# Optimization experiments

Measured on AMD Instinct MI355X. Metric: run time of the kernel, lower is better.

The kernel has to match this reference:

```python
import jax, jax.numpy as jnp
import numpy as np

N = 768
INPUT_DIM = 128
HIDDEN = 256
HEADS = 8
HEAD_DIM = HIDDEN // HEADS  # 32
SCALE = float(np.sqrt(HEAD_DIM))


def _linear_params(key, fan_in, fan_out):
    kw, kb = jax.random.split(key)
    lim = 1.0 / np.sqrt(fan_in)
    W = jax.random.uniform(kw, (fan_in, fan_out), jnp.float32, -lim, lim)
    b = jax.random.uniform(kb, (fan_out,), jnp.float32, -lim, lim)
    return W, b


def setup_inputs() -> dict:
    key = jax.random.key(0)
    ks = jax.random.split(key, 9)
    x = jax.random.normal(ks[0], (N, INPUT_DIM), jnp.float32)
    pos = jax.random.normal(ks[1], (N, 3), jnp.float32)
    Wq, bq = _linear_params(ks[2], INPUT_DIM, HIDDEN)
    Wk, bk = _linear_params(ks[3], INPUT_DIM, HIDDEN)
    Wv, bv = _linear_params(ks[4], INPUT_DIM, HIDDEN)
    Wo, bo = _linear_params(ks[5], HIDDEN, HIDDEN)
    W1, b1 = _linear_params(ks[6], 3, HIDDEN)
    W2, b2 = _linear_params(ks[7], HIDDEN, HIDDEN)
    W3, b3 = _linear_params(ks[8], HIDDEN, HEAD_DIM)
    return dict(x=x, pos=pos, Wq=Wq, bq=bq, Wk=Wk, bk=bk, Wv=Wv, bv=bv,
                Wo=Wo, bo=bo, W1=W1, b1=b1, W2=W2, b2=b2, W3=W3, b3=b3)


def reference(x, pos, Wq, bq, Wk, bk, Wv, bv, Wo, bo, W1, b1, W2, b2, W3, b3):
    n = x.shape[0]
    Q = (x @ Wq + bq).reshape(n, HEADS, HEAD_DIM)
    K = (x @ Wk + bk).reshape(n, HEADS, HEAD_DIM)
    V = (x @ Wv + bv).reshape(n, HEADS, HEAD_DIM)

    # rel_pos[i, j] = pos[j] - pos[i], shape (N, N, 3)
    rel = pos[None, :, :] - pos[:, None, :]
    h = jax.nn.relu(rel @ W1 + b1)          # (N, N, HIDDEN)
    h = jax.nn.relu(h @ W2 + b2)            # (N, N, HIDDEN)
    enc = h @ W3 + b3                        # (N, N, HEAD_DIM)

    scores = jnp.einsum('ihd,jhd->hij', Q, K) / SCALE
    scores = scores + jnp.einsum('ihd,ijd->hij', Q, enc) / SCALE
    attn = jax.nn.softmax(scores, axis=-1)   # (H, N, N); dropout is identity at eval
    out = jnp.einsum('hij,jhd->ihd', attn, V).reshape(n, HIDDEN)
    return out @ Wo + bo
```

## Files before the change

### kernel.cpp

```cpp
#include <hip/hip_runtime.h>
#include <hip/hip_bf16.h>

#define N 768
#define IN_DIM 128
#define HID 256
#define HD 32
#define TJ 64
#define NT (N / TJ)
#define NTH (NT / 2)
#define SCALE_INV 0.17677669529663687f

typedef short s16x8 __attribute__((ext_vector_type(8)));
typedef float f32x4 __attribute__((ext_vector_type(4)));

__device__ __forceinline__ float bf2f(unsigned short s) {
    return __uint_as_float(((unsigned)s) << 16);
}
__device__ __forceinline__ unsigned short bf_bits(float f) {
    __hip_bfloat16 h = __float2bfloat16(f);
    union { __hip_bfloat16 h; unsigned short u; } c; c.h = h; return c.u;
}
__device__ __forceinline__ unsigned cvt2(float a, float b) {
    __hip_bfloat162 h2 = __float22bfloat162_rn(make_float2(a, b));
    union { __hip_bfloat162 h; unsigned u; } c; c.h = h2; return c.u;
}

#define BAR_LDS() do { asm volatile("s_waitcnt lgkmcnt(0)" ::: "memory"); \
                       __builtin_amdgcn_s_barrier(); } while (0)

__global__ __launch_bounds__(256) void prep_kernel(
    const float* __restrict__ x, const float* __restrict__ pos,
    const float* __restrict__ Wq, const float* __restrict__ bq,
    const float* __restrict__ Wk, const float* __restrict__ bk,
    const float* __restrict__ Wv, const float* __restrict__ bv,
    const float* __restrict__ W1, const float* __restrict__ W2,
    const float* __restrict__ W3, const float* __restrict__ Wo,
    float* __restrict__ Q, float* __restrict__ Kt,
    unsigned short* __restrict__ Vt, float* __restrict__ A,
    unsigned short* __restrict__ w2f, float* __restrict__ WoT,
    unsigned short* __restrict__ w3qg)
{
    const int bx = blockIdx.x, t = threadIdx.x;
    __shared__ float xs[IN_DIM];
    __shared__ float ps[3];
    __shared__ float qrow[HID];

    if (bx >= N) {
        const int p = (bx - N) * 256 + t;
        const int e = p & 7, l = (p >> 3) & 63, nt = (p >> 9) & 15, s = p >> 13;
        const int krow = 32 * s + 8 * (l >> 4) + e;
        const int ncol = 16 * nt + (l & 15);
        w2f[p] = bf_bits(W2[krow * HID + ncol]);
        WoT[p] = Wo[(p & 255) * HID + (p >> 8)];
        return;
    }

    const int i = bx;
    if (t < IN_DIM) xs[t] = x[i * IN_DIM + t];
    if (t < 3) ps[t] = pos[i * 3 + t];
    __syncthreads();
    float q = bq[t], k = bk[t], v = bv[t];
#pragma unroll 8
    for (int kk = 0; kk < IN_DIM; ++kk) {
        const float xv = xs[kk];
        q += xv * Wq[kk * HID + t];
        k += xv * Wk[kk * HID + t];
        v += xv * Wv[kk * HID + t];
    }
    const float a = ps[0] * W1[t] + ps[1] * W1[HID + t] + ps[2] * W1[2 * HID + t];
    Q[i * HID + t] = q;
    Kt[(size_t)t * N + i] = k;
    Vt[(size_t)t * N + i] = bf_bits(v);
    A[i * HID + t] = a;
    qrow[t] = q;
    __syncthreads();

    const int l = t & 63, sp = t >> 6, lg = l >> 4, hh = l & 15;
#pragma unroll
    for (int ss = 0; ss < 2; ++ss) {
        const int s = 2 * sp + ss;
        s16x8 frag = {0, 0, 0, 0, 0, 0, 0, 0};
        if (hh < 8) {
#pragma unroll
            for (int e = 0; e < 8; ++e) {
                const int kk = 32 * s + 8 * lg + e;
                const float* w3p = W3 + kk * HD;
                float acc = 0.f;
#pragma unroll
                for (int d0 = 0; d0 < 32; d0 += 4) {
                    const float4 wv = *(const float4*)(w3p + d0);
                    acc += wv.x * qrow[hh * HD + d0] + wv.y * qrow[hh * HD + d0 + 1]
                         + wv.z * qrow[hh * HD + d0 + 2] + wv.w * qrow[hh * HD + d0 + 3];
                }
                frag[e] = (short)bf_bits(acc);
            }
        }
        *(s16x8*)(w3qg + (size_t)i * 4096 + (size_t)(s * 64 + l) * 8) = frag;
    }
}

__global__ __launch_bounds__(256) void s1_kernel(
    const float* __restrict__ Q, const float* __restrict__ Kt,
    float* __restrict__ S1)
{
    const int t = threadIdx.x;
    const int i0 = (blockIdx.x / 12) * 32;
    const int j0 = (blockIdx.x % 12) * 64;
    __shared__ float qTs[256 * 36];

    {
        const int iq = t & 31;
        const int dbase = (t >> 5) * 32;
        const int xk = t >> 5;
        const int colsw = (((iq >> 2) ^ xk) << 2) + (iq & 3);
        const float* qp = Q + (size_t)(i0 + iq) * HID + dbase;
#pragma unroll
        for (int cc = 0; cc < 8; ++cc) {
            const float4 qv = *(const float4*)(qp + 4 * cc);
            qTs[(dbase + 4 * cc + 0) * 36 + colsw] = qv.x;
            qTs[(dbase + 4 * cc + 1) * 36 + colsw] = qv.y;
            qTs[(dbase + 4 * cc + 2) * 36 + colsw] = qv.z;
            qTs[(dbase + 4 * cc + 3) * 36 + colsw] = qv.w;
        }
    }
    __syncthreads();

    const int h = t >> 5, jj = t & 31;
    const int j1 = j0 + jj, j2 = j0 + jj + 32;
    f32x4 acc0[8] = {}, acc1[8] = {};
    const float* kp = Kt + (size_t)(32 * h) * N + j1;
#pragma unroll 4
    for (int d = 0; d < 32; ++d) {
        const float k0 = kp[(size_t)d * N];
        const float k1 = kp[(size_t)d * N + 32];
        const float* qrow = &qTs[(32 * h + d) * 36];
#pragma unroll
        for (int ic = 0; ic < 8; ++ic) {
            const f32x4 qv = *(const f32x4*)&qrow[(ic ^ h) << 2];
            acc0[ic] += qv * k0;
            acc1[ic] += qv * k1;
        }
    }
    float* op = S1 + (size_t)h * (N * N) + (size_t)i0 * N;
#pragma unroll
    for (int ic = 0; ic < 8; ++ic)
#pragma unroll
        for (int u = 0; u < 4; ++u) {
            op[(size_t)(4 * ic + u) * N + j1] = acc0[ic][u];
            op[(size_t)(4 * ic + u) * N + j2] = acc1[ic][u];
        }
}

__global__ __launch_bounds__(256, 2) void fused_main_kernel(
    const float* __restrict__ Ag, const float* __restrict__ S1,
    const unsigned short* __restrict__ Vt,
    const unsigned short* __restrict__ w2fg, const unsigned short* __restrict__ w3qg,
    const float* __restrict__ b1, const float* __restrict__ b2,
    float* __restrict__ pv0g, float* __restrict__ pv1g,
    float* __restrict__ psump, float* __restrict__ mp)
{
    const int bid = blockIdx.x;
    const int i = bid >> 1, jhalf = bid & 1;
    const int t = threadIdx.x;
    const int w = t >> 6, l = t & 63;
    const int lg = l >> 4, l15 = l & 15;

    __shared__ __align__(16) short h1f[4 * 8 * 64 * 8];
    __shared__ __align__(16) short h2s[64 * 264];
    __shared__ __align__(16) short w3qf[8 * 64 * 8];
    __shared__ __align__(16) float slds[8 * 68];
    __shared__ __align__(16) float plds[8 * 68];
    __shared__ float basek[HID];
    __shared__ float hm[8], hpsum[8], hresc[8];

    basek[t] = b1[t] - Ag[(size_t)i * HID + t];
    {
        const int c0 = t, c1 = t + 256;
        *(s16x8*)&w3qf[c0 * 8] = *(const s16x8*)(w3qg + (size_t)i * 4096 + (size_t)c0 * 8);
        *(s16x8*)&w3qf[c1 * 8] = *(const s16x8*)(w3qg + (size_t)i * 4096 + (size_t)c1 * 8);
    }
    if (t < 8) { hm[t] = -3.0e38f; hpsum[t] = 0.f; }
    float bias[4];
#pragma unroll
    for (int n = 0; n < 4; ++n) bias[n] = b2[64 * w + 16 * n + l15];

    float pv = 0.f;
    const int hsel = w + ((l >> 5) << 2);
    const int hid2 = hsel * 32 + (l & 31);
    const unsigned short* vrow = Vt + (size_t)hid2 * N;
    BAR_LDS();

#pragma unroll 1
    for (int tt = 0; tt < NTH; ++tt) {
        const int j0 = (jhalf * NTH + tt) * TJ;

        const int jj = 16 * w + l15;
        const float* ap = Ag + (size_t)(j0 + jj) * HID + 8 * lg;
#pragma unroll
        for (int s = 0; s < 8; ++s) {
            const float4 a0 = *(const float4*)(ap + 32 * s);
            const float4 a1 = *(const float4*)(ap + 32 * s + 4);
            const float4 c0 = *(const float4*)&basek[32 * s + 8 * lg];
            const float4 c4 = *(const float4*)&basek[32 * s + 8 * lg + 4];
            uint4 hv;
            hv.x = cvt2(fmaxf(a0.x + c0.x, 0.f), fmaxf(a0.y + c0.y, 0.f));
            hv.y = cvt2(fmaxf(a0.z + c0.z, 0.f), fmaxf(a0.w + c0.w, 0.f));
            hv.z = cvt2(fmaxf(a1.x + c4.x, 0.f), fmaxf(a1.y + c4.y, 0.f));
            hv.w = cvt2(fmaxf(a1.z + c4.z, 0.f), fmaxf(a1.w + c4.w, 0.f));
            *(uint4*)&h1f[((w * 8 + s) * 64 + l) * 8] = hv;
        }
        float4 s1v = make_float4(0.f, 0.f, 0.f, 0.f);
        if (l15 < 8)
            s1v = *(const float4*)(S1 + (size_t)l15 * (N * N) + (size_t)i * N
                                   + j0 + 16 * w + 4 * lg);
        s16x8 bfr[32];
#pragma unroll
        for (int s = 0; s < 8; ++s)
#pragma unroll
            for (int n = 0; n < 4; ++n)
                bfr[s * 4 + n] = *(const s16x8*)(w2fg +
                    (size_t)(((s * 16 + 4 * w + n) * 64 + l)) * 8);
        BAR_LDS();

#pragma unroll
        for (int mt = 0; mt < 4; ++mt) {
            s16x8 a[8];
#pragma unroll
            for (int s = 0; s < 8; ++s)
                a[s] = *(const s16x8*)&h1f[((mt * 8 + s) * 64 + l) * 8];
#pragma unroll
            for (int n = 0; n < 4; ++n) {
                f32x4 acc = {bias[n], bias[n], bias[n], bias[n]};
#pragma unroll
                for (int s = 0; s < 8; ++s)
                    acc = __builtin_amdgcn_mfma_f32_16x16x32_bf16(a[s], bfr[s * 4 + n], acc, 0, 0, 0);
                const int col = 64 * w + 16 * n + l15;
                const int jrow = 16 * mt + 4 * lg;
#pragma unroll
                for (int r = 0; r < 4; ++r)
                    h2s[(jrow + r) * 264 + col] = (short)bf_bits(fmaxf(acc[r], 0.f));
            }
        }
        BAR_LDS();

        f32x4 acc2 = {};
#pragma unroll
        for (int s = 0; s < 8; ++s) {
            const s16x8 a2 = *(const s16x8*)&h2s[(16 * w + l15) * 264 + 32 * s + 8 * lg];
            const s16x8 wq = *(const s16x8*)&w3qf[(s * 64 + l) * 8];
            acc2 = __builtin_amdgcn_mfma_f32_16x16x32_bf16(a2, wq, acc2, 0, 0, 0);
        }
        if (l15 < 8) {
            float4 sc;
            sc.x = (acc2[0] + s1v.x) * SCALE_INV;
            sc.y = (acc2[1] + s1v.y) * SCALE_INV;
            sc.z = (acc2[2] + s1v.z) * SCALE_INV;
            sc.w = (acc2[3] + s1v.w) * SCALE_INV;
            *(float4*)&slds[l15 * 68 + 16 * w + 4 * lg] = sc;
        }
        BAR_LDS();

        s16x8 vv[8];
        {
            const unsigned short* vp = vrow + j0;
#pragma unroll
            for (int c = 0; c < 8; ++c) vv[c] = *(const s16x8*)(vp + c * 8);
        }

        {
            const int h0 = w, h1 = w + 4;
            const float s0 = slds[h0 * 68 + l];
            const float s1 = slds[h1 * 68 + l];
            float m0 = s0, m1 = s1;
#pragma unroll
            for (int o = 1; o < 64; o <<= 1) {
                m0 = fmaxf(m0, __shfl_xor(m0, o));
                m1 = fmaxf(m1, __shfl_xor(m1, o));
            }
            const float M0 = hm[h0], M1 = hm[h1];
            const float nm0 = fmaxf(M0, m0), nm1 = fmaxf(M1, m1);
            const float p0 = __expf(s0 - nm0), p1 = __expf(s1 - nm1);
            plds[h0 * 68 + l] = p0;
            plds[h1 * 68 + l] = p1;
            float t0 = p0, t1 = p1;
#pragma unroll
            for (int o = 1; o < 64; o <<= 1) {
                t0 += __shfl_xor(t0, o);
                t1 += __shfl_xor(t1, o);
            }
            if (l == 0) {
                const float r0 = __expf(M0 - nm0), r1 = __expf(M1 - nm1);
                hresc[h0] = r0; hresc[h1] = r1;
                hpsum[h0] = hpsum[h0] * r0 + t0;
                hpsum[h1] = hpsum[h1] * r1 + t1;
                hm[h0] = nm0; hm[h1] = nm1;
            }
        }
        asm volatile("s_waitcnt lgkmcnt(0)" ::: "memory");

        {
            pv *= hresc[hsel];
            const float* pp = &plds[hsel * 68];
#pragma unroll
            for (int c = 0; c < 8; ++c) {
                const s16x8 vvv = vv[c];
                const float4 pa = *(const float4*)(pp + 8 * c);
                const float4 pb = *(const float4*)(pp + 8 * c + 4);
                pv += pa.x * bf2f((unsigned short)vvv[0]) + pa.y * bf2f((unsigned short)vvv[1])
                    + pa.z * bf2f((unsigned short)vvv[2]) + pa.w * bf2f((unsigned short)vvv[3])
                    + pb.x * bf2f((unsigned short)vvv[4]) + pb.y * bf2f((unsigned short)vvv[5])
                    + pb.z * bf2f((unsigned short)vvv[6]) + pb.w * bf2f((unsigned short)vvv[7]);
            }
        }
    }

    float* pvb = jhalf ? pv1g : pv0g;
    pvb[(size_t)i * HID + hid2] = pv;
    BAR_LDS();
    if (t < 8) {
        psump[(size_t)bid * 8 + t] = hpsum[t];
        mp[(size_t)bid * 8 + t] = hm[t];
    }
}

__global__ __launch_bounds__(256) void combine_kernel(
    const float* __restrict__ pv0g, const float* __restrict__ pv1g,
    const float* __restrict__ psump, const float* __restrict__ mp,
    const float* __restrict__ WoT, const float* __restrict__ bo,
    float* __restrict__ out)
{
    const int i = blockIdx.x, t = threadIdx.x;
    const int h = t >> 5;
    __shared__ float oa[HID];

    const float m0 = mp[(size_t)(2 * i) * 8 + h];
    const float m1 = mp[(size_t)(2 * i + 1) * 8 + h];
    const float ms = fmaxf(m0, m1);
    const float e0 = __expf(m0 - ms), e1 = __expf(m1 - ms);
    const float num = pv0g[(size_t)i * HID + t] * e0 + pv1g[(size_t)i * HID + t] * e1;
    const float den = psump[(size_t)(2 * i) * 8 + h] * e0
                    + psump[(size_t)(2 * i + 1) * 8 + h] * e1;
    oa[t] = num / den;
    __syncthreads();

    float r = bo[t];
    const float* wop = WoT + (size_t)t * HID;
#pragma unroll 4
    for (int k = 0; k < HID; k += 4) {
        const float4 ov = *(const float4*)&oa[k];
        const float4 wv = *(const float4*)(wop + k);
        r += ov.x * wv.x + ov.y * wv.y + ov.z * wv.z + ov.w * wv.w;
    }
    out[(size_t)i * HID + t] = r;
}

extern "C" void kernel_launch(void* const* d_in, const int* in_sizes, int n_in,
                              void* d_out, int out_size, void* d_ws, size_t ws_size,
                              hipStream_t stream)
{
    const float* x   = (const float*)d_in[0];
    const float* pos = (const float*)d_in[1];
    const float* Wq  = (const float*)d_in[2];
    const float* bq  = (const float*)d_in[3];
    const float* Wk  = (const float*)d_in[4];
    const float* bk  = (const float*)d_in[5];
    const float* Wv  = (const float*)d_in[6];
    const float* bv  = (const float*)d_in[7];
    const float* Wo  = (const float*)d_in[8];
    const float* bo  = (const float*)d_in[9];
    const float* W1  = (const float*)d_in[10];
    const float* b1  = (const float*)d_in[11];
    const float* W2  = (const float*)d_in[12];
    const float* b2  = (const float*)d_in[13];
    const float* W3  = (const float*)d_in[14];
    const float* b3  = (const float*)d_in[15];
    (void)b3;
    float* out = (float*)d_out;

    char* ws = (char*)d_ws;
    float* Q  = (float*)(ws + 0);
    float* A  = (float*)(ws + 786432);
    float* Kt = (float*)(ws + 1572864);
    unsigned short* Vtb = (unsigned short*)(ws + 2359296);
    float* S1 = (float*)(ws + 2752512);
    unsigned short* w2f  = (unsigned short*)(ws + 21626880);
    unsigned short* w3qg = (unsigned short*)(ws + 21757952);
    float* WoT = (float*)(ws + 28049408);
    float* pv0g  = (float*)(ws + 0);
    float* pv1g  = (float*)(ws + 1572864);
    float* psump = (float*)(ws + 28311552);
    float* mp    = (float*)(ws + 28360704);

    prep_kernel<<<1024, 256, 0, stream>>>(x, pos, Wq, bq, Wk, bk, Wv, bv,
                                          W1, W2, W3, Wo,
                                          Q, Kt, Vtb, A, w2f, WoT, w3qg);
    s1_kernel<<<288, 256, 0, stream>>>(Q, Kt, S1);
    fused_main_kernel<<<2 * N, 256, 0, stream>>>(A, S1, Vtb, w2f, w3qg,
                                                 b1, b2, pv0g, pv1g, psump, mp);
    combine_kernel<<<N, 256, 0, stream>>>(pv0g, pv1g, psump, mp, WoT, bo, out);
}
```

Measured before the change: 209.3 us.

## Fuse QK score computation into main kernel, drop S1 buffer and kernel

Removes the separate s1_kernel that wrote a full H×N×N fp32 score tensor (about 18 MB) to global memory and read it back in the main kernel. Each main-kernel tile now computes the Q·K dot products itself from a row-major K copy and the query row staged in LDS, then passes them through slds. K is stored row-major so the per-row dot product reads contiguous memory. This removes the large global round trip and one launch, at the cost of extra FMA and K loads inside the main loop, and it reuses slds, which the later store must not overwrite too early.

```diff
diff --git a/kernel.cpp b/kernel.cpp
--- a/kernel.cpp
+++ b/kernel.cpp
@@ -35,7 +35,7 @@
     const float* __restrict__ Wv, const float* __restrict__ bv,
     const float* __restrict__ W1, const float* __restrict__ W2,
     const float* __restrict__ W3, const float* __restrict__ Wo,
-    float* __restrict__ Q, float* __restrict__ Kt,
+    float* __restrict__ Q, float* __restrict__ Krm,
     unsigned short* __restrict__ Vt, float* __restrict__ A,
     unsigned short* __restrict__ w2f, float* __restrict__ WoT,
     unsigned short* __restrict__ w3qg)
@@ -69,7 +69,7 @@
     }
     const float a = ps[0] * W1[t] + ps[1] * W1[HID + t] + ps[2] * W1[2 * HID + t];
     Q[i * HID + t] = q;
-    Kt[(size_t)t * N + i] = k;
+    Krm[(size_t)i * HID + t] = k;
     Vt[(size_t)t * N + i] = bf_bits(v);
     A[i * HID + t] = a;
     qrow[t] = q;
@@ -99,61 +99,9 @@
     }
 }
 
-__global__ __launch_bounds__(256) void s1_kernel(
-    const float* __restrict__ Q, const float* __restrict__ Kt,
-    float* __restrict__ S1)
-{
-    const int t = threadIdx.x;
-    const int i0 = (blockIdx.x / 12) * 32;
-    const int j0 = (blockIdx.x % 12) * 64;
-    __shared__ float qTs[256 * 36];
-
-    {
-        const int iq = t & 31;
-        const int dbase = (t >> 5) * 32;
-        const int xk = t >> 5;
-        const int colsw = (((iq >> 2) ^ xk) << 2) + (iq & 3);
-        const float* qp = Q + (size_t)(i0 + iq) * HID + dbase;
-#pragma unroll
-        for (int cc = 0; cc < 8; ++cc) {
-            const float4 qv = *(const float4*)(qp + 4 * cc);
-            qTs[(dbase + 4 * cc + 0) * 36 + colsw] = qv.x;
-            qTs[(dbase + 4 * cc + 1) * 36 + colsw] = qv.y;
-            qTs[(dbase + 4 * cc + 2) * 36 + colsw] = qv.z;
-            qTs[(dbase + 4 * cc + 3) * 36 + colsw] = qv.w;
-        }
-    }
-    __syncthreads();
-
-    const int h = t >> 5, jj = t & 31;
-    const int j1 = j0 + jj, j2 = j0 + jj + 32;
-    f32x4 acc0[8] = {}, acc1[8] = {};
-    const float* kp = Kt + (size_t)(32 * h) * N + j1;
-#pragma unroll 4
-    for (int d = 0; d < 32; ++d) {
-        const float k0 = kp[(size_t)d * N];
-        const float k1 = kp[(size_t)d * N + 32];
-        const float* qrow = &qTs[(32 * h + d) * 36];
-#pragma unroll
-        for (int ic = 0; ic < 8; ++ic) {
-            const f32x4 qv = *(const f32x4*)&qrow[(ic ^ h) << 2];
-            acc0[ic] += qv * k0;
-            acc1[ic] += qv * k1;
-        }
-    }
-    float* op = S1 + (size_t)h * (N * N) + (size_t)i0 * N;
-#pragma unroll
-    for (int ic = 0; ic < 8; ++ic)
-#pragma unroll
-        for (int u = 0; u < 4; ++u) {
-            op[(size_t)(4 * ic + u) * N + j1] = acc0[ic][u];
-            op[(size_t)(4 * ic + u) * N + j2] = acc1[ic][u];
-        }
-}
-
 __global__ __launch_bounds__(256, 2) void fused_main_kernel(
-    const float* __restrict__ Ag, const float* __restrict__ S1,
-    const unsigned short* __restrict__ Vt,
+    const float* __restrict__ Ag, const float* __restrict__ Qg,
+    const float* __restrict__ Krm, const unsigned short* __restrict__ Vt,
     const unsigned short* __restrict__ w2fg, const unsigned short* __restrict__ w3qg,
     const float* __restrict__ b1, const float* __restrict__ b2,
     float* __restrict__ pv0g, float* __restrict__ pv1g,
@@ -171,9 +119,11 @@
     __shared__ __align__(16) float slds[8 * 68];
     __shared__ __align__(16) float plds[8 * 68];
     __shared__ float basek[HID];
+    __shared__ float qs[HID];
     __shared__ float hm[8], hpsum[8], hresc[8];
 
     basek[t] = b1[t] - Ag[(size_t)i * HID + t];
+    qs[t] = Qg[(size_t)i * HID + t];
     {
         const int c0 = t, c1 = t + 256;
         *(s16x8*)&w3qf[c0 * 8] = *(const s16x8*)(w3qg + (size_t)i * 4096 + (size_t)c0 * 8);
@@ -188,6 +138,8 @@
     const int hsel = w + ((l >> 5) << 2);
     const int hid2 = hsel * 32 + (l & 31);
     const unsigned short* vrow = Vt + (size_t)hid2 * N;
+    const int jjq = t >> 2;
+    const int hq = 2 * (t & 3);
     BAR_LDS();
 
 #pragma unroll 1
@@ -209,10 +161,23 @@
             hv.w = cvt2(fmaxf(a1.z + c4.z, 0.f), fmaxf(a1.w + c4.w, 0.f));
             *(uint4*)&h1f[((w * 8 + s) * 64 + l) * 8] = hv;
         }
-        float4 s1v = make_float4(0.f, 0.f, 0.f, 0.f);
-        if (l15 < 8)
-            s1v = *(const float4*)(S1 + (size_t)l15 * (N * N) + (size_t)i * N
-                                   + j0 + 16 * w + 4 * lg);
+        float qk0 = 0.f, qk1 = 0.f;
+        {
+            const float* kp = Krm + (size_t)(j0 + jjq) * HID + 32 * hq;
+            const float* qp = &qs[32 * hq];
+#pragma unroll
+            for (int c = 0; c < 8; ++c) {
+                const float4 kv = *(const float4*)(kp + 4 * c);
+                const float4 qv = *(const float4*)(qp + 4 * c);
+                qk0 += kv.x * qv.x + kv.y * qv.y + kv.z * qv.z + kv.w * qv.w;
+            }
+#pragma unroll
+            for (int c = 0; c < 8; ++c) {
+                const float4 kv = *(const float4*)(kp + 32 + 4 * c);
+                const float4 qv = *(const float4*)(qp + 32 + 4 * c);
+                qk1 += kv.x * qv.x + kv.y * qv.y + kv.z * qv.z + kv.w * qv.w;
+            }
+        }
         s16x8 bfr[32];
 #pragma unroll
         for (int s = 0; s < 8; ++s)
@@ -222,6 +187,9 @@
                     (size_t)(((s * 16 + 4 * w + n) * 64 + l)) * 8);
         BAR_LDS();
 
+        slds[hq * 68 + jjq] = qk0;
+        slds[(hq + 1) * 68 + jjq] = qk1;
+
 #pragma unroll
         for (int mt = 0; mt < 4; ++mt) {
             s16x8 a[8];
@@ -243,6 +211,9 @@
         }
         BAR_LDS();
 
+        float4 s1v = make_float4(0.f, 0.f, 0.f, 0.f);
+        if (l15 < 8)
+            s1v = *(const float4*)&slds[l15 * 68 + 16 * w + 4 * lg];
         f32x4 acc2 = {};
 #pragma unroll
         for (int s = 0; s < 8; ++s) {
@@ -378,24 +349,22 @@
     float* out = (float*)d_out;
 
     char* ws = (char*)d_ws;
-    float* Q  = (float*)(ws + 0);
-    float* A  = (float*)(ws + 786432);
-    float* Kt = (float*)(ws + 1572864);
+    float* Q   = (float*)(ws + 0);
+    float* A   = (float*)(ws + 786432);
+    float* Krm = (float*)(ws + 1572864);
     unsigned short* Vtb = (unsigned short*)(ws + 2359296);
-    float* S1 = (float*)(ws + 2752512);
-    unsigned short* w2f  = (unsigned short*)(ws + 21626880);
-    unsigned short* w3qg = (unsigned short*)(ws + 21757952);
-    float* WoT = (float*)(ws + 28049408);
-    float* pv0g  = (float*)(ws + 0);
-    float* pv1g  = (float*)(ws + 1572864);
-    float* psump = (float*)(ws + 28311552);
-    float* mp    = (float*)(ws + 28360704);
+    unsigned short* w2f  = (unsigned short*)(ws + 2752512);
+    unsigned short* w3qg = (unsigned short*)(ws + 2883584);
+    float* WoT   = (float*)(ws + 9175040);
+    float* pv0g  = (float*)(ws + 9437184);
+    float* pv1g  = (float*)(ws + 10223616);
+    float* psump = (float*)(ws + 11010048);
+    float* mp    = (float*)(ws + 11059200);
 
     prep_kernel<<<1024, 256, 0, stream>>>(x, pos, Wq, bq, Wk, bk, Wv, bv,
                                           W1, W2, W3, Wo,
-                                          Q, Kt, Vtb, A, w2f, WoT, w3qg);
-    s1_kernel<<<288, 256, 0, stream>>>(Q, Kt, S1);
-    fused_main_kernel<<<2 * N, 256, 0, stream>>>(A, S1, Vtb, w2f, w3qg,
+                                          Q, Krm, Vtb, A, w2f, WoT, w3qg);
+    fused_main_kernel<<<2 * N, 256, 0, stream>>>(A, Q, Krm, Vtb, w2f, w3qg,
                                                  b1, b2, pv0g, pv1g, psump, mp);
     combine_kernel<<<N, 256, 0, stream>>>(pv0g, pv1g, psump, mp, WoT, bo, out);
 }
```

Measured after the change: 255.2 us. +21.9%, slower.
